# Kernel optimization log

Measured on AMD Instinct MI355X. Metric: run time of the kernel, lower is better.

The kernel has to match this reference:

```python
import jax, jax.numpy as jnp
import numpy as np

B, S, H = 2, 2048, 1024
NH, HD = 16, 64
SCALE = HD ** -0.5


def setup_inputs() -> dict:
    key = jax.random.key(0)
    k1, k2, k3, k4 = jax.random.split(key, 4)
    hidden_states = jax.random.normal(k1, (B, S, H), dtype=jnp.float32)
    attention_mask = jax.random.randint(k2, (B, S), 0, 2, dtype=jnp.int32)
    # xavier-uniform-ish init scale
    w_qkv = jax.random.normal(k3, (3 * H, H), dtype=jnp.float32) * (2.0 / (H + 3 * H)) ** 0.5
    w_out = jax.random.normal(k4, (H, H), dtype=jnp.float32) * (1.0 / H) ** 0.5
    return {"hidden_states": hidden_states, "attention_mask": attention_mask,
            "w_qkv": w_qkv, "w_out": w_out}


def reference(hidden_states, attention_mask, w_qkv, w_out):
    b, s, _ = hidden_states.shape
    qkv = hidden_states @ w_qkv.T                      # [B,S,3H]
    q, k, v = jnp.split(qkv, 3, axis=-1)
    # [B,S,H] -> [B,NH,S,HD]
    reshape = lambda x: x.reshape(b, s, NH, HD).transpose(0, 2, 1, 3)
    q, k, v = reshape(q), reshape(k), reshape(v)
    scores = jnp.einsum('bhqd,bhkd->bhqk', q, k) * SCALE   # [B,NH,S,S]
    mask = attention_mask[:, None, None, :] == 0           # [B,1,1,S]
    scores = jnp.where(mask, -jnp.inf, scores)
    attn = jax.nn.softmax(scores, axis=-1)                 # dropout p: eval mode -> identity
    out = jnp.einsum('bhqk,bhkd->bhqd', attn, v)           # [B,NH,S,HD]
    out = out.transpose(0, 2, 1, 3).reshape(b, s, H)
    return out @ w_out.T
```

## Files before the change

### kernel.cpp

```cpp
#include <hip/hip_runtime.h>
#include <string.h>


typedef __bf16    bf16x8 __attribute__((ext_vector_type(8)));
typedef _Float16  f16x4  __attribute__((ext_vector_type(4)));
typedef _Float16  f16x2  __attribute__((ext_vector_type(2)));
typedef float     f32x4  __attribute__((ext_vector_type(4)));

#define NTOK   4096
#define HDIM   1024
#define SEQ    2048
#define NHEAD  16
#define F2SHIFT 4.0f
#define QSCALE  0.18033688f
#define LSTRIDE 68
#define TSTRIDE 66

__device__ __forceinline__ float bf2f(unsigned short u) {
    union { unsigned int i; float f; } x;
    x.i = ((unsigned int)u) << 16;
    return x.f;
}
__device__ __forceinline__ unsigned short f2bf(float f) {
    union { __bf16 h; unsigned short u; } x;
    x.h = (__bf16)f;
    return x.u;
}
__device__ __forceinline__ unsigned short f2h(float f) {
    union { _Float16 h; unsigned short u; } x;
    x.h = (_Float16)f;
    return x.u;
}
__device__ __forceinline__ f16x2 pkrtz(float a, float b) {
    union { __fp16 __attribute__((ext_vector_type(2))) i; f16x2 o; } x;
    x.i = __builtin_amdgcn_cvt_pkrtz(a, b);
    return x.o;
}

__device__ __forceinline__ int detect_f32(const unsigned short* hs) {
    unsigned int idx = (threadIdx.x & 63) * 4096u;
    float f = bf2f(hs[idx]);
    return __any(!(fabsf(f) < 1e4f));
}

typedef const __attribute__((address_space(1))) unsigned int* gptr_u32;
typedef __attribute__((address_space(3))) unsigned int* lptr_u32;

__device__ __forceinline__ void async16(const unsigned short* g, unsigned short* l) {
    __builtin_amdgcn_global_load_lds((gptr_u32)g, (lptr_u32)l, 16, 0, 0);
}

__global__ void convert3_kernel(const void* __restrict__ s0, const void* __restrict__ s1,
                                const void* __restrict__ s2, unsigned short* __restrict__ dst) {
    const int isf32 = detect_f32((const unsigned short*)s0);
    if (!isf32) return;
    int g = blockIdx.x * blockDim.x + threadIdx.x;
    const int stride = gridDim.x * blockDim.x;
    for (; g < 1048576; g += stride) {
        int i = g * 8;
        const void* src; int off;
        if (i < 4194304)      { src = s0; off = i; }
        else if (i < 7340032) { src = s1; off = i - 4194304; }
        else                  { src = s2; off = i - 7340032; }
        const float* s = (const float*)src + off;
        unsigned short o[8];
#pragma unroll
        for (int j = 0; j < 8; j++) o[j] = f2bf(s[j]);
        *(uint4*)(dst + i) = *(const uint4*)o;
    }
}

__global__ __launch_bounds__(256) void gemm_qkv(
    const unsigned short* __restrict__ Xc, const unsigned short* __restrict__ Wc,
    const unsigned short* __restrict__ Xraw, const unsigned short* __restrict__ Wraw,
    unsigned short* __restrict__ q_out, unsigned short* __restrict__ k_out,
    unsigned short* __restrict__ v_out) {
    const int K = 1024;
    __shared__ __align__(16) unsigned short Xs[128 * 32];
    __shared__ __align__(16) unsigned short Ws[128 * 32];
    __shared__ __align__(16) unsigned short Tr[128 * TSTRIDE];

    const int isf32 = detect_f32(Xraw);
    const unsigned short* X = isf32 ? Xc : Xraw;
    const unsigned short* W = isf32 ? Wc : Wraw;

    const int t = threadIdx.x;
    const int w = t >> 6, lane = t & 63, quad = lane >> 4, lr = lane & 15;
    const int wrow = (w >> 1) * 64, wcol = (w & 1) * 64;
    const int m0 = blockIdx.y * 128, n0 = blockIdx.x * 128;
    const bool vblk = (n0 >= 2048);

    f32x4 acc[4][4];
#pragma unroll
    for (int mi = 0; mi < 4; mi++)
#pragma unroll
        for (int ni = 0; ni < 4; ni++) acc[mi][ni] = (f32x4){0.f, 0.f, 0.f, 0.f};

    const int srow = w * 32 + (lane >> 2);
    const int scol = (lane & 3) * 8;
    const unsigned short* xg = X + (size_t)(m0 + srow) * K + scol;
    const unsigned short* wg = W + (size_t)(n0 + srow) * K + scol;
    unsigned short* xl0 = &Xs[w * 1024];
    unsigned short* wl0 = &Ws[w * 1024];

    for (int k0 = 0; k0 < K; k0 += 32) {
        __syncthreads();
        async16(xg + k0, xl0);
        async16(xg + k0 + 16 * K, xl0 + 512);
        async16(wg + k0, wl0);
        async16(wg + k0 + 16 * K, wl0 + 512);
        __syncthreads();
        bf16x8 af[4], bfr[4];
#pragma unroll
        for (int mi = 0; mi < 4; mi++)
            af[mi] = *(bf16x8*)&Xs[(wrow + mi * 16 + lr) * 32 + quad * 8];
#pragma unroll
        for (int ni = 0; ni < 4; ni++)
            bfr[ni] = *(bf16x8*)&Ws[(wcol + ni * 16 + lr) * 32 + quad * 8];
        if (!vblk) {
#pragma unroll
            for (int mi = 0; mi < 4; mi++)
#pragma unroll
                for (int ni = 0; ni < 4; ni++)
                    acc[mi][ni] = __builtin_amdgcn_mfma_f32_16x16x32_bf16(af[mi], bfr[ni], acc[mi][ni], 0, 0, 0);
        } else {
#pragma unroll
            for (int mi = 0; mi < 4; mi++)
#pragma unroll
                for (int ni = 0; ni < 4; ni++)
                    acc[mi][ni] = __builtin_amdgcn_mfma_f32_16x16x32_bf16(bfr[ni], af[mi], acc[mi][ni], 0, 0, 0);
        }
    }

    if (!vblk) {
        const int isQ = (n0 < 1024);
        unsigned short* outp = isQ ? q_out : k_out;
#pragma unroll
        for (int pass = 0; pass < 2; pass++) {
            __syncthreads();
            if ((wcol >> 6) == pass) {
#pragma unroll
                for (int mi = 0; mi < 4; mi++)
#pragma unroll
                    for (int ni = 0; ni < 4; ni++)
#pragma unroll
                        for (int rr = 0; rr < 4; rr++) {
                            int r = wrow + mi * 16 + quad * 4 + rr;
                            int c = ni * 16 + lr;
                            float val = acc[mi][ni][rr];
                            Tr[r * TSTRIDE + c] = isQ ? f2bf(val * QSCALE) : f2bf(val);
                        }
            }
            __syncthreads();
            int nh = ((n0 + pass * 64) & 1023) >> 6;
#pragma unroll
            for (int it = 0; it < 4; it++) {
                int r = (t >> 3) + it * 32;
                int c8 = (t & 7) * 8;
                uint4 v = *(uint4*)&Tr[r * TSTRIDE + c8];
                int mrow = m0 + r;
                int bb = mrow >> 11, s = mrow & 2047;
                *(uint4*)&outp[((size_t)(bb * NHEAD + nh) * SEQ + s) * 64 + c8] = v;
            }
        }
    } else {
#pragma unroll
        for (int pass = 0; pass < 2; pass++) {
            __syncthreads();
            if ((wrow >> 6) == pass) {
#pragma unroll
                for (int mi = 0; mi < 4; mi++)
#pragma unroll
                    for (int ni = 0; ni < 4; ni++)
#pragma unroll
                        for (int rr = 0; rr < 4; rr++) {
                            int cn = wcol + ni * 16 + quad * 4 + rr;
                            int tk = mi * 16 + lr;
                            Tr[cn * TSTRIDE + tk] = f2h(acc[mi][ni][rr]);
                        }
            }
            __syncthreads();
#pragma unroll
            for (int it = 0; it < 4; it++) {
                int cn = (t >> 3) + it * 32;
                int tk8 = (t & 7) * 8;
                uint4 v = *(uint4*)&Tr[cn * TSTRIDE + tk8];
                int rem = (n0 + cn) & 1023;
                int nh = rem >> 6, hd = rem & 63;
                int m = m0 + pass * 64 + tk8;
                int bb = m >> 11, s = m & 2047;
                *(uint4*)&v_out[((size_t)(bb * NHEAD + nh) * 64 + hd) * SEQ + s] = v;
            }
        }
    }
}

__global__ __launch_bounds__(256) void gemm_out(
    const unsigned short* __restrict__ X, const unsigned short* __restrict__ Wc,
    const unsigned short* __restrict__ Wraw,
    void* __restrict__ d_out, const unsigned short* __restrict__ hs_raw) {
    const int K = 1024, N = 1024;
    __shared__ __align__(16) unsigned short Xs[64 * 32];
    __shared__ __align__(16) unsigned short Ws[128 * 32];

    const int isf32 = detect_f32(hs_raw);
    const unsigned short* W = isf32 ? Wc : Wraw;

    const int t = threadIdx.x;
    const int w = t >> 6, lane = t & 63, quad = lane >> 4, lr = lane & 15;
    const int wrow = (w >> 1) * 32, wcol = (w & 1) * 64;
    const int m0 = blockIdx.y * 64, n0 = blockIdx.x * 128;

    f32x4 acc[2][4];
#pragma unroll
    for (int mi = 0; mi < 2; mi++)
#pragma unroll
        for (int ni = 0; ni < 4; ni++) acc[mi][ni] = (f32x4){0.f, 0.f, 0.f, 0.f};

    const int sxrow = w * 16 + (lane >> 2);
    const int swrow = w * 32 + (lane >> 2);
    const int scol = (lane & 3) * 8;
    const unsigned short* xg = X + (size_t)(m0 + sxrow) * K + scol;
    const unsigned short* wg = W + (size_t)(n0 + swrow) * K + scol;
    unsigned short* xl0 = &Xs[w * 512];
    unsigned short* wl0 = &Ws[w * 1024];

    for (int k0 = 0; k0 < K; k0 += 32) {
        __syncthreads();
        async16(xg + k0, xl0);
        async16(wg + k0, wl0);
        async16(wg + k0 + 16 * K, wl0 + 512);
        __syncthreads();
        bf16x8 af[2], bfr[4];
#pragma unroll
        for (int mi = 0; mi < 2; mi++)
            af[mi] = *(bf16x8*)&Xs[(wrow + mi * 16 + lr) * 32 + quad * 8];
#pragma unroll
        for (int ni = 0; ni < 4; ni++)
            bfr[ni] = *(bf16x8*)&Ws[(wcol + ni * 16 + lr) * 32 + quad * 8];
#pragma unroll
        for (int mi = 0; mi < 2; mi++)
#pragma unroll
            for (int ni = 0; ni < 4; ni++)
                acc[mi][ni] = __builtin_amdgcn_mfma_f32_16x16x32_bf16(af[mi], bfr[ni], acc[mi][ni], 0, 0, 0);
    }

#pragma unroll
    for (int mi = 0; mi < 2; mi++)
#pragma unroll
        for (int ni = 0; ni < 4; ni++)
#pragma unroll
            for (int rr = 0; rr < 4; rr++) {
                int mrow = m0 + wrow + mi * 16 + quad * 4 + rr;
                int j = n0 + wcol + ni * 16 + lr;
                float val = acc[mi][ni][rr];
                size_t dst = (size_t)mrow * N + j;
                if (isf32) ((float*)d_out)[dst] = val;
                else ((unsigned short*)d_out)[dst] = f2bf(val);
            }
}

__global__ __launch_bounds__(256) void flash_attn_v8(
    const unsigned short* __restrict__ q, const unsigned short* __restrict__ k,
    const unsigned short* __restrict__ vt, const int* __restrict__ mask,
    unsigned short* __restrict__ attn_out) {
    __shared__ __align__(16) unsigned short Ks[64 * LSTRIDE];
    __shared__ __align__(16) unsigned short Vt[64 * LSTRIDE];
    __shared__ __align__(16) float Msk[80];

    const int t = threadIdx.x;
    const int w = t >> 6, lane = t & 63, quad = lane >> 4, lr = lane & 15;
    const int bh = blockIdx.x, b = bh >> 4, h = bh & 15;
    const int q0 = blockIdx.y * 128;

    const unsigned short* qb = q + (size_t)bh * SEQ * 64;
    const unsigned short* kb = k + (size_t)bh * SEQ * 64;
    const unsigned short* vtb = vt + (size_t)bh * 64 * SEQ;
    const int* mb = mask + b * SEQ;

    bf16x8 qf[2][2];
#pragma unroll
    for (int qg = 0; qg < 2; qg++) {
        const unsigned short* qrow = qb + (size_t)(q0 + w * 32 + qg * 16 + lr) * 64 + quad * 8;
        qf[qg][0] = *(const bf16x8*)qrow;
        qf[qg][1] = *(const bf16x8*)(qrow + 32);
    }

    f32x4 oacc[2][4];
#pragma unroll
    for (int qg = 0; qg < 2; qg++)
#pragma unroll
        for (int dt = 0; dt < 4; dt++) oacc[qg][dt] = (f32x4){0.f, 0.f, 0.f, 0.f};
    float l_st[2] = {0.f, 0.f};

    const int sr = t >> 2;
    const int sc = (t & 3) * 16;

    for (int kk0 = 0; kk0 < SEQ; kk0 += 64) {
        const uint4* kp = (const uint4*)(kb + (size_t)(kk0 + sr) * 64 + sc);
        const uint4* vp = (const uint4*)(vtb + (size_t)sr * SEQ + kk0 + sc);
        uint4 ka = kp[0], kb2 = kp[1];
        uint4 va = vp[0], vb2 = vp[1];
        float mval = 0.f;
        if (t < 64) mval = (mb[kk0 + t] == 0) ? -1e30f : -F2SHIFT;

        __syncthreads();
        *(uint4*)&Ks[sr * LSTRIDE + sc] = ka;
        *(uint4*)&Ks[sr * LSTRIDE + sc + 8] = kb2;
        *(uint4*)&Vt[sr * LSTRIDE + sc] = va;
        *(uint4*)&Vt[sr * LSTRIDE + sc + 8] = vb2;
        if (t < 64) Msk[t] = mval;
        __syncthreads();

#pragma unroll
        for (int mt = 0; mt < 4; mt++) {
            bf16x8 a1h0 = *(bf16x8*)&Ks[(mt * 16 + lr) * LSTRIDE + quad * 8];
            bf16x8 a1h1 = *(bf16x8*)&Ks[(mt * 16 + lr) * LSTRIDE + 32 + quad * 8];
            f16x4 a2[4];
#pragma unroll
            for (int dt = 0; dt < 4; dt++)
                a2[dt] = *(f16x4*)&Vt[(dt * 16 + lr) * LSTRIDE + mt * 16 + quad * 4];
            float4 mv = *(const float4*)&Msk[mt * 16 + quad * 4];

#pragma unroll
            for (int qg = 0; qg < 2; qg++) {
                f32x4 z = (f32x4){mv.x, mv.y, mv.z, mv.w};
                z = __builtin_amdgcn_mfma_f32_16x16x32_bf16(a1h0, qf[qg][0], z, 0, 0, 0);
                z = __builtin_amdgcn_mfma_f32_16x16x32_bf16(a1h1, qf[qg][1], z, 0, 0, 0);
                float p0 = __builtin_amdgcn_exp2f(z[0]);
                float p1 = __builtin_amdgcn_exp2f(z[1]);
                float p2 = __builtin_amdgcn_exp2f(z[2]);
                float p3 = __builtin_amdgcn_exp2f(z[3]);
                l_st[qg] += (p0 + p1) + (p2 + p3);
                f16x2 ab = pkrtz(p0, p1);
                f16x2 cd = pkrtz(p2, p3);
                f16x4 b2;
                b2[0] = ab[0]; b2[1] = ab[1]; b2[2] = cd[0]; b2[3] = cd[1];
#pragma unroll
                for (int dt = 0; dt < 4; dt++)
                    oacc[qg][dt] = __builtin_amdgcn_mfma_f32_16x16x16f16(a2[dt], b2, oacc[qg][dt], 0, 0, 0);
            }
        }
    }

    float inv[2];
#pragma unroll
    for (int qg = 0; qg < 2; qg++) {
        float s = l_st[qg];
        s += __shfl_xor(s, 16);
        s += __shfl_xor(s, 32);
        inv[qg] = 1.0f / s;
    }
#pragma unroll
    for (int qg = 0; qg < 2; qg++) {
        size_t tok = (size_t)(b * SEQ + q0 + w * 32 + qg * 16 + lr);
#pragma unroll
        for (int dt = 0; dt < 4; dt++)
#pragma unroll
            for (int rr = 0; rr < 4; rr++)
                attn_out[tok * HDIM + h * 64 + dt * 16 + quad * 4 + rr] =
                    f2bf(oacc[qg][dt][rr] * inv[qg]);
    }
}

extern "C" void kernel_launch(void* const* d_in, const int* in_sizes, int n_in,
                              void* d_out, int out_size, void* d_ws, size_t ws_size,
                              hipStream_t stream) {
    const void* hs_raw = d_in[0];
    const int* mask = (const int*)d_in[1];
    const void* wqkv_raw = d_in[2];
    const void* wout_raw = d_in[3];

    char* wsb = (char*)d_ws;
    unsigned short* hs_c = (unsigned short*)(wsb + 256);
    unsigned short* wqkv_c = hs_c + 4194304;
    unsigned short* wout_c = wqkv_c + 3145728;
    unsigned short* qw = wout_c + 1048576;
    unsigned short* kw = qw + 4194304;
    unsigned short* vtw = kw + 4194304;
    unsigned short* ao = vtw + 4194304;

    convert3_kernel<<<256, 256, 0, stream>>>(hs_raw, wqkv_raw, wout_raw, hs_c);

    gemm_qkv<<<dim3(24, 32), 256, 0, stream>>>(hs_c, wqkv_c,
                                               (const unsigned short*)hs_raw,
                                               (const unsigned short*)wqkv_raw,
                                               qw, kw, vtw);
    flash_attn_v8<<<dim3(32, 16), 256, 0, stream>>>(qw, kw, vtw, mask, ao);
    gemm_out<<<dim3(8, 64), 256, 0, stream>>>(ao, wout_c,
                                              (const unsigned short*)wout_raw, d_out,
                                              (const unsigned short*)hs_raw);
}
```

Baseline: 197.8 us.

## Double GEMM K-tile depth and register-prefetch next K/V tile in flash attention

Both GEMM kernels now stage 64-wide K slices per iteration instead of 32, halving the number of barrier pairs and doing two MFMA sub-steps per staged tile. The QKV GEMM aliases its transpose buffer onto the input staging memory to keep shared memory usage bounded. The attention kernel loads the next K/V/mask tile into registers right after the LDS store, so global latency overlaps with the current tile's compute, at the cost of more live registers. The last iteration wraps around and prefetches a redundant tile.

```diff
diff --git a/kernel.cpp b/kernel.cpp
--- a/kernel.cpp
+++ b/kernel.cpp
@@ -76,9 +76,10 @@
     unsigned short* __restrict__ q_out, unsigned short* __restrict__ k_out,
     unsigned short* __restrict__ v_out) {
     const int K = 1024;
-    __shared__ __align__(16) unsigned short Xs[128 * 32];
-    __shared__ __align__(16) unsigned short Ws[128 * 32];
-    __shared__ __align__(16) unsigned short Tr[128 * TSTRIDE];
+    __shared__ __align__(16) char gsm[32768];
+    unsigned short* Xs = (unsigned short*)gsm;
+    unsigned short* Ws = (unsigned short*)(gsm + 16384);
+    unsigned short* Tr = (unsigned short*)gsm;
 
     const int isf32 = detect_f32(Xraw);
     const unsigned short* X = isf32 ? Xc : Xraw;
@@ -96,39 +97,43 @@
 #pragma unroll
         for (int ni = 0; ni < 4; ni++) acc[mi][ni] = (f32x4){0.f, 0.f, 0.f, 0.f};
 
-    const int srow = w * 32 + (lane >> 2);
-    const int scol = (lane & 3) * 8;
+    const int srow = w * 32 + (lane >> 3);
+    const int scol = (lane & 7) * 8;
     const unsigned short* xg = X + (size_t)(m0 + srow) * K + scol;
     const unsigned short* wg = W + (size_t)(n0 + srow) * K + scol;
-    unsigned short* xl0 = &Xs[w * 1024];
-    unsigned short* wl0 = &Ws[w * 1024];
-
-    for (int k0 = 0; k0 < K; k0 += 32) {
-        __syncthreads();
-        async16(xg + k0, xl0);
-        async16(xg + k0 + 16 * K, xl0 + 512);
-        async16(wg + k0, wl0);
-        async16(wg + k0 + 16 * K, wl0 + 512);
-        __syncthreads();
-        bf16x8 af[4], bfr[4];
-#pragma unroll
-        for (int mi = 0; mi < 4; mi++)
-            af[mi] = *(bf16x8*)&Xs[(wrow + mi * 16 + lr) * 32 + quad * 8];
-#pragma unroll
-        for (int ni = 0; ni < 4; ni++)
-            bfr[ni] = *(bf16x8*)&Ws[(wcol + ni * 16 + lr) * 32 + quad * 8];
-        if (!vblk) {
+    unsigned short* xl0 = &Xs[w * 32 * 64];
+    unsigned short* wl0 = &Ws[w * 32 * 64];
+
+    for (int k0 = 0; k0 < K; k0 += 64) {
+        __syncthreads();
+#pragma unroll
+        for (int j = 0; j < 4; j++) {
+            async16(xg + k0 + (size_t)j * 8 * K, xl0 + j * 512);
+            async16(wg + k0 + (size_t)j * 8 * K, wl0 + j * 512);
+        }
+        __syncthreads();
+#pragma unroll
+        for (int kw = 0; kw < 2; kw++) {
+            bf16x8 af[4], bfr[4];
 #pragma unroll
             for (int mi = 0; mi < 4; mi++)
-#pragma unroll
-                for (int ni = 0; ni < 4; ni++)
-                    acc[mi][ni] = __builtin_amdgcn_mfma_f32_16x16x32_bf16(af[mi], bfr[ni], acc[mi][ni], 0, 0, 0);
-        } else {
-#pragma unroll
-            for (int mi = 0; mi < 4; mi++)
-#pragma unroll
-                for (int ni = 0; ni < 4; ni++)
-                    acc[mi][ni] = __builtin_amdgcn_mfma_f32_16x16x32_bf16(bfr[ni], af[mi], acc[mi][ni], 0, 0, 0);
+                af[mi] = *(bf16x8*)&Xs[(wrow + mi * 16 + lr) * 64 + kw * 32 + quad * 8];
+#pragma unroll
+            for (int ni = 0; ni < 4; ni++)
+                bfr[ni] = *(bf16x8*)&Ws[(wcol + ni * 16 + lr) * 64 + kw * 32 + quad * 8];
+            if (!vblk) {
+#pragma unroll
+                for (int mi = 0; mi < 4; mi++)
+#pragma unroll
+                    for (int ni = 0; ni < 4; ni++)
+                        acc[mi][ni] = __builtin_amdgcn_mfma_f32_16x16x32_bf16(af[mi], bfr[ni], acc[mi][ni], 0, 0, 0);
+            } else {
+#pragma unroll
+                for (int mi = 0; mi < 4; mi++)
+#pragma unroll
+                    for (int ni = 0; ni < 4; ni++)
+                        acc[mi][ni] = __builtin_amdgcn_mfma_f32_16x16x32_bf16(bfr[ni], af[mi], acc[mi][ni], 0, 0, 0);
+            }
         }
     }
 
@@ -200,8 +205,8 @@
     const unsigned short* __restrict__ Wraw,
     void* __restrict__ d_out, const unsigned short* __restrict__ hs_raw) {
     const int K = 1024, N = 1024;
-    __shared__ __align__(16) unsigned short Xs[64 * 32];
-    __shared__ __align__(16) unsigned short Ws[128 * 32];
+    __shared__ __align__(16) unsigned short Xs[64 * 64];
+    __shared__ __align__(16) unsigned short Ws[128 * 64];
 
     const int isf32 = detect_f32(hs_raw);
     const unsigned short* W = isf32 ? Wc : Wraw;
@@ -217,32 +222,38 @@
 #pragma unroll
         for (int ni = 0; ni < 4; ni++) acc[mi][ni] = (f32x4){0.f, 0.f, 0.f, 0.f};
 
-    const int sxrow = w * 16 + (lane >> 2);
-    const int swrow = w * 32 + (lane >> 2);
-    const int scol = (lane & 3) * 8;
+    const int sxrow = w * 16 + (lane >> 3);
+    const int swrow = w * 32 + (lane >> 3);
+    const int scol = (lane & 7) * 8;
     const unsigned short* xg = X + (size_t)(m0 + sxrow) * K + scol;
     const unsigned short* wg = W + (size_t)(n0 + swrow) * K + scol;
-    unsigned short* xl0 = &Xs[w * 512];
-    unsigned short* wl0 = &Ws[w * 1024];
-
-    for (int k0 = 0; k0 < K; k0 += 32) {
-        __syncthreads();
-        async16(xg + k0, xl0);
-        async16(wg + k0, wl0);
-        async16(wg + k0 + 16 * K, wl0 + 512);
-        __syncthreads();
-        bf16x8 af[2], bfr[4];
-#pragma unroll
-        for (int mi = 0; mi < 2; mi++)
-            af[mi] = *(bf16x8*)&Xs[(wrow + mi * 16 + lr) * 32 + quad * 8];
-#pragma unroll
-        for (int ni = 0; ni < 4; ni++)
-            bfr[ni] = *(bf16x8*)&Ws[(wcol + ni * 16 + lr) * 32 + quad * 8];
-#pragma unroll
-        for (int mi = 0; mi < 2; mi++)
+    unsigned short* xl0 = &Xs[w * 16 * 64];
+    unsigned short* wl0 = &Ws[w * 32 * 64];
+
+    for (int k0 = 0; k0 < K; k0 += 64) {
+        __syncthreads();
+#pragma unroll
+        for (int j = 0; j < 2; j++)
+            async16(xg + k0 + (size_t)j * 8 * K, xl0 + j * 512);
+#pragma unroll
+        for (int j = 0; j < 4; j++)
+            async16(wg + k0 + (size_t)j * 8 * K, wl0 + j * 512);
+        __syncthreads();
+#pragma unroll
+        for (int kw = 0; kw < 2; kw++) {
+            bf16x8 af[2], bfr[4];
+#pragma unroll
+            for (int mi = 0; mi < 2; mi++)
+                af[mi] = *(bf16x8*)&Xs[(wrow + mi * 16 + lr) * 64 + kw * 32 + quad * 8];
 #pragma unroll
             for (int ni = 0; ni < 4; ni++)
-                acc[mi][ni] = __builtin_amdgcn_mfma_f32_16x16x32_bf16(af[mi], bfr[ni], acc[mi][ni], 0, 0, 0);
+                bfr[ni] = *(bf16x8*)&Ws[(wcol + ni * 16 + lr) * 64 + kw * 32 + quad * 8];
+#pragma unroll
+            for (int mi = 0; mi < 2; mi++)
+#pragma unroll
+                for (int ni = 0; ni < 4; ni++)
+                    acc[mi][ni] = __builtin_amdgcn_mfma_f32_16x16x32_bf16(af[mi], bfr[ni], acc[mi][ni], 0, 0, 0);
+        }
     }
 
 #pragma unroll
@@ -260,7 +271,7 @@
             }
 }
 
-__global__ __launch_bounds__(256) void flash_attn_v8(
+__global__ __launch_bounds__(256) void flash_attn_v9(
     const unsigned short* __restrict__ q, const unsigned short* __restrict__ k,
     const unsigned short* __restrict__ vt, const int* __restrict__ mask,
     unsigned short* __restrict__ attn_out) {
@@ -296,14 +307,14 @@
     const int sr = t >> 2;
     const int sc = (t & 3) * 16;
 
+    uint4 ka = *(const uint4*)(kb + (size_t)sr * 64 + sc);
+    uint4 kb2 = *(const uint4*)(kb + (size_t)sr * 64 + sc + 8);
+    uint4 va = *(const uint4*)(vtb + (size_t)sr * SEQ + sc);
+    uint4 vb2 = *(const uint4*)(vtb + (size_t)sr * SEQ + sc + 8);
+    float mval = 0.f;
+    if (t < 64) mval = (mb[t] == 0) ? -1e30f : -F2SHIFT;
+
     for (int kk0 = 0; kk0 < SEQ; kk0 += 64) {
-        const uint4* kp = (const uint4*)(kb + (size_t)(kk0 + sr) * 64 + sc);
-        const uint4* vp = (const uint4*)(vtb + (size_t)sr * SEQ + kk0 + sc);
-        uint4 ka = kp[0], kb2 = kp[1];
-        uint4 va = vp[0], vb2 = vp[1];
-        float mval = 0.f;
-        if (t < 64) mval = (mb[kk0 + t] == 0) ? -1e30f : -F2SHIFT;
-
         __syncthreads();
         *(uint4*)&Ks[sr * LSTRIDE + sc] = ka;
         *(uint4*)&Ks[sr * LSTRIDE + sc + 8] = kb2;
@@ -311,6 +322,17 @@
         *(uint4*)&Vt[sr * LSTRIDE + sc + 8] = vb2;
         if (t < 64) Msk[t] = mval;
         __syncthreads();
+
+        {
+            int kk1 = (kk0 + 64) & (SEQ - 1);
+            const uint4* kp = (const uint4*)(kb + (size_t)(kk1 + sr) * 64 + sc);
+            const uint4* vp = (const uint4*)(vtb + (size_t)sr * SEQ + kk1 + sc);
+            ka = kp[0];
+            kb2 = *(const uint4*)(kb + (size_t)(kk1 + sr) * 64 + sc + 8);
+            va = vp[0];
+            vb2 = *(const uint4*)(vtb + (size_t)sr * SEQ + kk1 + sc + 8);
+            if (t < 64) mval = (mb[kk1 + t] == 0) ? -1e30f : -F2SHIFT;
+        }
 
 #pragma unroll
         for (int mt = 0; mt < 4; mt++) {
@@ -386,7 +408,7 @@
                                                (const unsigned short*)hs_raw,
                                                (const unsigned short*)wqkv_raw,
                                                qw, kw, vtw);
-    flash_attn_v8<<<dim3(32, 16), 256, 0, stream>>>(qw, kw, vtw, mask, ao);
+    flash_attn_v9<<<dim3(32, 16), 256, 0, stream>>>(qw, kw, vtw, mask, ao);
     gemm_out<<<dim3(8, 64), 256, 0, stream>>>(ao, wout_c,
                                               (const unsigned short*)wout_raw, d_out,
                                               (const unsigned short*)hs_raw);
```

After: 203.5 us. +2.9%, slower.
